# Performance work log

Measured on AMD Instinct MI355X. Metric: run time of the kernel, lower is better.

The kernel has to match this reference:

```python
import jax, jax.numpy as jnp
import numpy as np

B, S, E = 4, 2048, 1024
H, D = 16, 64

def setup_inputs() -> dict:
    key = jax.random.key(0)
    kx, kq, ko = jax.random.split(key, 3)
    scale_in = 1.0 / np.sqrt(E)
    scale_hd = 1.0 / np.sqrt(H * D)
    x = jax.random.normal(kx, (B, S, E), dtype=jnp.float32)
    W_qkv = jax.random.normal(kq, (E, 3, H, D), dtype=jnp.float32) * scale_in
    b_qkv = jnp.zeros((3, H, D), dtype=jnp.float32)
    W_out = jax.random.normal(ko, (H, D, E), dtype=jnp.float32) * scale_hd
    b_out = jnp.zeros((E,), dtype=jnp.float32)
    return {"x": x, "W_qkv": W_qkv, "b_qkv": b_qkv, "W_out": W_out, "b_out": b_out}

def reference(x, W_qkv, b_qkv, W_out, b_out):
    # QKV projection: [B,S,E] x [E,3,H,D] -> [B,S,3,H,D]
    qkv = jnp.einsum('bse,ethd->bsthd', x, W_qkv) + b_qkv
    q, k, v = qkv[:, :, 0], qkv[:, :, 1], qkv[:, :, 2]  # [B,S,H,D]
    # scores: [B,H,S(query),S(key)]
    scores = jnp.einsum('bqhd,bkhd->bhqk', q, k) / jnp.sqrt(jnp.float32(D))
    pos_q = jnp.arange(S)[:, None]
    pos_k = jnp.arange(S)[None, :]
    causal_mask = (pos_q >= pos_k).astype(scores.dtype)  # [S,S]
    scores = scores - 1e9 * (1.0 - causal_mask)
    weights = jax.nn.softmax(scores, axis=-1)
    # dropout is identity in inference mode
    answers = jnp.einsum('bhqk,bkhd->bqhd', weights, v)  # [B,S,H,D]
    out = jnp.einsum('bqhd,hde->bqe', answers, W_out) + b_out
    return out
```

## Files before the change

kernel.cpp:

```cpp
#include <hip/hip_runtime.h>
#include <math.h>

#define B_ 4
#define S_ 2048
#define E_ 1024
#define H_ 16
#define D_ 64

typedef _Float16 half8v __attribute__((ext_vector_type(8)));
typedef _Float16 half4v __attribute__((ext_vector_type(4)));
typedef __attribute__((ext_vector_type(4))) float f32x4;

__global__ __launch_bounds__(256)
void convert_f32_f16_kernel(const float* __restrict__ in, _Float16* __restrict__ out, int n4)
{
    const int i = blockIdx.x * 256 + threadIdx.x;
    if (i < n4) {
        float4 v = ((const float4*)in)[i];
        half4v h;
        h[0] = (_Float16)v.x; h[1] = (_Float16)v.y;
        h[2] = (_Float16)v.z; h[3] = (_Float16)v.w;
        ((half4v*)out)[i] = h;
    }
}

__global__ __launch_bounds__(256, 4)
void transpose_f32_f16_kernel(const float* __restrict__ in, _Float16* __restrict__ out,
                              int R, int C)
{
    __shared__ float tile[64][65];
    const int r0 = blockIdx.x * 64, c0 = blockIdx.y * 64;
    const int tr = threadIdx.x >> 6, tc = threadIdx.x & 63;
#pragma unroll
    for (int i = 0; i < 16; ++i)
        tile[i * 4 + tr][tc] = in[(size_t)(r0 + i * 4 + tr) * C + c0 + tc];
    __syncthreads();
#pragma unroll
    for (int i = 0; i < 16; ++i)
        out[(size_t)(c0 + i * 4 + tr) * R + r0 + tc] = (_Float16)tile[tc][i * 4 + tr];
}

__device__ __forceinline__ void gemm_core_f16(
    const _Float16* __restrict__ A, const _Float16* __restrict__ Bt,
    int bm, int bn, int tid,
    _Float16* As, _Float16* Bs,
    f32x4 (&acc)[4][4])
{
    const int K = 1024;
    const int lane = tid & 63;
    const int l15 = lane & 15, g = lane >> 4;
    const int w = tid >> 6;
    const int wm = (w >> 1) * 64, wn = (w & 1) * 64;
    const int swl = l15 & 7;

    const int sr = tid >> 3;
    const int sk = tid & 7;

    const _Float16* Ab = A + (size_t)(bm * 128) * K;
    const _Float16* Bb = Bt + (size_t)(bn * 128) * K;

    half8v arg[4], brg[4];
#pragma unroll
    for (int it = 0; it < 4; ++it) {
        arg[it] = *(const half8v*)(Ab + (size_t)(it * 32 + sr) * K + sk * 8);
        brg[it] = *(const half8v*)(Bb + (size_t)(it * 32 + sr) * K + sk * 8);
    }

    for (int k0 = 0; k0 < K; k0 += 64) {
        __syncthreads();
#pragma unroll
        for (int it = 0; it < 4; ++it) {
            const int r = it * 32 + sr;
            const int off = r * 64 + (sk ^ (r & 7)) * 8;
            *(half8v*)&As[off] = arg[it];
            *(half8v*)&Bs[off] = brg[it];
        }
        __syncthreads();
        if (k0 + 64 < K) {
#pragma unroll
            for (int it = 0; it < 4; ++it) {
                arg[it] = *(const half8v*)(Ab + (size_t)(it * 32 + sr) * K + k0 + 64 + sk * 8);
                brg[it] = *(const half8v*)(Bb + (size_t)(it * 32 + sr) * K + k0 + 64 + sk * 8);
            }
        }
#pragma unroll
        for (int kk = 0; kk < 2; ++kk) {
            const int slot = (kk * 4 + g) ^ swl;
            half8v af[4];
#pragma unroll
            for (int fm = 0; fm < 4; ++fm)
                af[fm] = *(const half8v*)&As[(wm + fm * 16 + l15) * 64 + slot * 8];
#pragma unroll
            for (int fn = 0; fn < 4; ++fn) {
                half8v bf = *(const half8v*)&Bs[(wn + fn * 16 + l15) * 64 + slot * 8];
#pragma unroll
                for (int fm = 0; fm < 4; ++fm)
                    acc[fm][fn] = __builtin_amdgcn_mfma_f32_16x16x32_f16(
                        af[fm], bf, acc[fm][fn], 0, 0, 0);
            }
        }
    }
}

__global__ __launch_bounds__(256, 2)
void gemm_qkv_f16_kernel(const _Float16* __restrict__ Xh, const _Float16* __restrict__ Wqh,
                         const float* __restrict__ bias,
                         _Float16* __restrict__ qf, _Float16* __restrict__ kf,
                         _Float16* __restrict__ vf)
{
    __shared__ _Float16 As[128 * 64], Bs[128 * 64];
    const int tid = threadIdx.x;
    const int bm = blockIdx.x, bn = blockIdx.y;

    f32x4 acc[4][4];
#pragma unroll
    for (int i = 0; i < 4; ++i)
#pragma unroll
        for (int j = 0; j < 4; ++j) acc[i][j] = f32x4{0.f, 0.f, 0.f, 0.f};

    gemm_core_f16(Xh, Wqh, bm, bn, tid, As, Bs, acc);

    const int lane = tid & 63;
    const int l15 = lane & 15, l4 = lane >> 4;
    const int w = tid >> 6;
    const int wm = (w >> 1) * 64, wn = (w & 1) * 64;

#pragma unroll
    for (int fn = 0; fn < 4; ++fn) {
        const int c = bn * 128 + wn + fn * 16 + l15;
        const float bv = bias[c];
        const int t = c >> 10;
        const int h = (c >> 6) & 15;
        const int d = c & 63;
        if (t < 2) {
            _Float16* dst = (t == 0) ? qf : kf;
#pragma unroll
            for (int fm = 0; fm < 4; ++fm) {
                const int rowb = bm * 128 + wm + fm * 16 + l4 * 4;
#pragma unroll
                for (int r = 0; r < 4; ++r) {
                    const int row = rowb + r;
                    const int b = row >> 11;
                    const int s = row & (S_ - 1);
                    dst[((size_t)(b * H_ + h) * S_ + s) * D_ + d] =
                        (_Float16)(acc[fm][fn][r] + bv);
                }
            }
        } else {
#pragma unroll
            for (int fm = 0; fm < 4; ++fm) {
                const int rowb = bm * 128 + wm + fm * 16 + l4 * 4;
                const int b = rowb >> 11;
                const int s0 = rowb & (S_ - 1);
                half4v pk;
#pragma unroll
                for (int r = 0; r < 4; ++r) pk[r] = (_Float16)(acc[fm][fn][r] + bv);
                *(half4v*)&vf[((size_t)(b * H_ + h) * D_ + d) * S_ + s0] = pk;
            }
        }
    }
}

__global__ __launch_bounds__(256, 4)
void flash_f16_kernel(const _Float16* __restrict__ qf, const _Float16* __restrict__ kf,
                      const _Float16* __restrict__ vf, _Float16* __restrict__ ansh)
{
    const int bh = blockIdx.y;
    const int b = bh >> 4, h = bh & 15;
    const int qb = (S_ / 64 - 1) - blockIdx.x;
    const int q0 = qb * 64;
    const int tid = threadIdx.x;
    const int lane = tid & 63;
    const int l15 = lane & 15, g = lane >> 4;
    const int w = tid >> 6;
    const int qrow = q0 + w * 16 + l15;
    const int swl = l15 & 7;

    __shared__ _Float16 Kh[64 * 64];
    __shared__ _Float16 Vth[64 * 64];

    half8v qh[2];
    {
        const _Float16* qp = qf + ((size_t)bh * S_ + qrow) * D_;
#pragma unroll
        for (int s = 0; s < 2; ++s) qh[s] = *(const half8v*)(qp + 32 * s + 8 * g);
    }

    f32x4 acc[4];
#pragma unroll
    for (int fd = 0; fd < 4; ++fd) acc[fd] = f32x4{0.f, 0.f, 0.f, 0.f};
    float m = -1e30f, lsum = 0.f;

    const int kp = tid & 63;
    const int kw = tid >> 6;
    const int vd = tid >> 2;
    const int vc = tid & 3;
    const int vbase = 32 * (vc >> 1) + 8 * (vc & 1);

    const _Float16* Kg = kf + (size_t)bh * S_ * D_;
    const _Float16* Vg = vf + ((size_t)bh * D_ + vd) * S_;

    const int nkv = qb + 1;

    half8v krA = *(const half8v*)(Kg + (size_t)kp * D_ + 16 * kw);
    half8v krB = *(const half8v*)(Kg + (size_t)kp * D_ + 16 * kw + 8);
    half8v vrA = *(const half8v*)(Vg + vbase);
    half8v vrB = *(const half8v*)(Vg + vbase + 16);

    for (int kb = 0; kb < nkv; ++kb) {
        const int k0 = kb * 64;
        __syncthreads();
        {
            const int o0 = kp * 64 + ((2 * kw) ^ (kp & 7)) * 8;
            const int o1 = kp * 64 + ((2 * kw + 1) ^ (kp & 7)) * 8;
            *(half8v*)&Kh[o0] = krA;
            *(half8v*)&Kh[o1] = krB;
            half8v c0, c1;
#pragma unroll
            for (int j = 0; j < 4; ++j) {
                c0[j] = vrA[j];     c0[4 + j] = vrB[j];
                c1[j] = vrA[4 + j]; c1[4 + j] = vrB[4 + j];
            }
            const int p0 = vd * 64 + ((2 * vc) ^ (vd & 7)) * 8;
            const int p1 = vd * 64 + ((2 * vc + 1) ^ (vd & 7)) * 8;
            *(half8v*)&Vth[p0] = c0;
            *(half8v*)&Vth[p1] = c1;
        }
        __syncthreads();
        if (kb + 1 < nkv) {
            const int kn = k0 + 64;
            krA = *(const half8v*)(Kg + (size_t)(kn + kp) * D_ + 16 * kw);
            krB = *(const half8v*)(Kg + (size_t)(kn + kp) * D_ + 16 * kw + 8);
            vrA = *(const half8v*)(Vg + kn + vbase);
            vrB = *(const half8v*)(Vg + kn + vbase + 16);
        }

        f32x4 qk[4];
#pragma unroll
        for (int f = 0; f < 4; ++f) qk[f] = f32x4{0.f, 0.f, 0.f, 0.f};
#pragma unroll
        for (int s = 0; s < 2; ++s) {
#pragma unroll
            for (int f = 0; f < 4; ++f) {
                const int off = (16 * f + l15) * 64 + ((4 * s + g) ^ swl) * 8;
                half8v kv = *(const half8v*)&Kh[off];
                qk[f] = __builtin_amdgcn_mfma_f32_16x16x32_f16(kv, qh[s], qk[f], 0, 0, 0);
            }
        }

        float p[4][4];
        float tmax = -1e30f;
#pragma unroll
        for (int f = 0; f < 4; ++f)
#pragma unroll
            for (int r = 0; r < 4; ++r) {
                const int kpos = k0 + 16 * f + 4 * g + r;
                float sv = qk[f][r] * 0.125f;
                sv = (kpos <= qrow) ? sv : -1e30f;
                p[f][r] = sv;
                tmax = fmaxf(tmax, sv);
            }
        tmax = fmaxf(tmax, __shfl_xor(tmax, 16));
        tmax = fmaxf(tmax, __shfl_xor(tmax, 32));
        const float mnew = fmaxf(m, tmax);
        const float corr = __expf(m - mnew);
#pragma unroll
        for (int fd = 0; fd < 4; ++fd) acc[fd] *= corr;
        float ls = 0.f;
#pragma unroll
        for (int f = 0; f < 4; ++f)
#pragma unroll
            for (int r = 0; r < 4; ++r) {
                const float e = __expf(p[f][r] - mnew);
                p[f][r] = e;
                ls += e;
            }
        ls += __shfl_xor(ls, 16);
        ls += __shfl_xor(ls, 32);
        lsum = lsum * corr + ls;
        m = mnew;

        half8v pb0, pb1;
#pragma unroll
        for (int j = 0; j < 4; ++j) {
            pb0[j]     = (_Float16)p[0][j];
            pb0[4 + j] = (_Float16)p[1][j];
            pb1[j]     = (_Float16)p[2][j];
            pb1[4 + j] = (_Float16)p[3][j];
        }

#pragma unroll
        for (int t = 0; t < 2; ++t) {
            const half8v pb = t ? pb1 : pb0;
#pragma unroll
            for (int fd = 0; fd < 4; ++fd) {
                const int off = (16 * fd + l15) * 64 + ((4 * t + g) ^ swl) * 8;
                half8v vv = *(const half8v*)&Vth[off];
                acc[fd] = __builtin_amdgcn_mfma_f32_16x16x32_f16(vv, pb, acc[fd], 0, 0, 0);
            }
        }
    }

    const float inv = 1.f / lsum;
    _Float16* dst = ansh + ((size_t)(b * S_ + qrow) * H_ + h) * D_;
#pragma unroll
    for (int fd = 0; fd < 4; ++fd) {
        half4v o4;
#pragma unroll
        for (int r = 0; r < 4; ++r) o4[r] = (_Float16)(acc[fd][r] * inv);
        *(half4v*)&dst[16 * fd + 4 * g] = o4;
    }
}

__global__ __launch_bounds__(256, 2)
void gemm_out_f16_kernel(const _Float16* __restrict__ Ah, const _Float16* __restrict__ Woh,
                         const float* __restrict__ bias, float* __restrict__ out)
{
    __shared__ _Float16 As[128 * 64], Bs[128 * 64];
    const int tid = threadIdx.x;
    const int bm = blockIdx.x, bn = blockIdx.y;

    f32x4 acc[4][4];
#pragma unroll
    for (int i = 0; i < 4; ++i)
#pragma unroll
        for (int j = 0; j < 4; ++j) acc[i][j] = f32x4{0.f, 0.f, 0.f, 0.f};

    gemm_core_f16(Ah, Woh, bm, bn, tid, As, Bs, acc);

    const int lane = tid & 63;
    const int l15 = lane & 15, l4 = lane >> 4;
    const int w = tid >> 6;
    const int wm = (w >> 1) * 64, wn = (w & 1) * 64;

#pragma unroll
    for (int fn = 0; fn < 4; ++fn) {
        const int c = bn * 128 + wn + fn * 16 + l15;
        const float bv = bias[c];
#pragma unroll
        for (int fm = 0; fm < 4; ++fm) {
            const int rowb = bm * 128 + wm + fm * 16 + l4 * 4;
#pragma unroll
            for (int r = 0; r < 4; ++r)
                out[(size_t)(rowb + r) * E_ + c] = acc[fm][fn][r] + bv;
        }
    }
}

extern "C" void kernel_launch(void* const* d_in, const int* in_sizes, int n_in,
                              void* d_out, int out_size, void* d_ws, size_t ws_size,
                              hipStream_t stream) {
    const float* x     = (const float*)d_in[0];
    const float* W_qkv = (const float*)d_in[1];
    const float* b_qkv = (const float*)d_in[2];
    const float* W_out = (const float*)d_in[3];
    const float* b_out = (const float*)d_in[4];
    float* out = (float*)d_out;

    const size_t N1 = (size_t)B_ * H_ * S_ * D_;
    const size_t MK = (size_t)8192 * 1024;
    const size_t WQ = (size_t)3072 * 1024;
    const size_t WO = (size_t)1024 * 1024;
    const size_t need = (MK + WQ + WO + 4 * N1) * sizeof(_Float16);
    if (ws_size < need) return;

    _Float16* Xh   = (_Float16*)d_ws;
    _Float16* Wqh  = Xh + MK;
    _Float16* Woh  = Wqh + WQ;
    _Float16* qf   = Woh + WO;
    _Float16* kf   = qf + N1;
    _Float16* vf   = kf + N1;
    _Float16* ansh = vf + N1;

    convert_f32_f16_kernel<<<(int)(MK / 4 / 256), 256, 0, stream>>>(x, Xh, (int)(MK / 4));
    transpose_f32_f16_kernel<<<dim3(16, 48), 256, 0, stream>>>(W_qkv, Wqh, 1024, 3072);
    transpose_f32_f16_kernel<<<dim3(16, 16), 256, 0, stream>>>(W_out, Woh, 1024, 1024);

    gemm_qkv_f16_kernel<<<dim3(64, 24), 256, 0, stream>>>(Xh, Wqh, b_qkv, qf, kf, vf);
    flash_f16_kernel<<<dim3(S_ / 64, B_ * H_), 256, 0, stream>>>(qf, kf, vf, ansh);
    gemm_out_f16_kernel<<<dim3(64, 8), 256, 0, stream>>>(ansh, Woh, b_out, out);
}
```

Measured before the change: 304.2 us.

## Pair causal query blocks per workgroup and double-buffer K/V tiles in flash kernel

Each flash-attention workgroup now handles two query blocks, j and 31-j, so every block does the same amount of causal work and each K/V tile loaded into shared memory is reused by both. K/V staging becomes double-buffered with one barrier per iteration. The online softmax skips rescaling when the new max rises by at most 8, and MFMA sections get raised wave priority. The costs are twice as many accumulator registers, double the LDS use, and a grid of only 1024 blocks, which could hurt occupancy.

```diff
diff --git a/kernel.cpp b/kernel.cpp
--- a/kernel.cpp
+++ b/kernel.cpp
@@ -161,35 +161,123 @@
     }
 }
 
+__device__ __forceinline__ void attn_tile(
+    const _Float16* __restrict__ Kb, const _Float16* __restrict__ Vb,
+    const half8v (&qh)[2], f32x4 (&acc)[4],
+    float& m, float& lsum,
+    int k0, int qrow, int l15, int g, int swl)
+{
+    f32x4 qk[4];
+#pragma unroll
+    for (int f = 0; f < 4; ++f) qk[f] = f32x4{0.f, 0.f, 0.f, 0.f};
+    __builtin_amdgcn_s_setprio(1);
+#pragma unroll
+    for (int s = 0; s < 2; ++s) {
+#pragma unroll
+        for (int f = 0; f < 4; ++f) {
+            const int off = (16 * f + l15) * 64 + ((4 * s + g) ^ swl) * 8;
+            half8v kv = *(const half8v*)&Kb[off];
+            qk[f] = __builtin_amdgcn_mfma_f32_16x16x32_f16(kv, qh[s], qk[f], 0, 0, 0);
+        }
+    }
+    __builtin_amdgcn_s_setprio(0);
+
+    float p[4][4];
+    float tmax = -1e30f;
+#pragma unroll
+    for (int f = 0; f < 4; ++f)
+#pragma unroll
+        for (int r = 0; r < 4; ++r) {
+            const int kpos = k0 + 16 * f + 4 * g + r;
+            float sv = qk[f][r] * 0.125f;
+            sv = (kpos <= qrow) ? sv : -1e30f;
+            p[f][r] = sv;
+            tmax = fmaxf(tmax, sv);
+        }
+    tmax = fmaxf(tmax, __shfl_xor(tmax, 16));
+    tmax = fmaxf(tmax, __shfl_xor(tmax, 32));
+
+    if (__ballot(tmax <= m + 8.f) != ~0ull) {
+        const float mnew = fmaxf(m, tmax);
+        const float corr = __expf(m - mnew);
+#pragma unroll
+        for (int fd = 0; fd < 4; ++fd) acc[fd] *= corr;
+        lsum *= corr;
+        m = mnew;
+    }
+    float ls = 0.f;
+#pragma unroll
+    for (int f = 0; f < 4; ++f)
+#pragma unroll
+        for (int r = 0; r < 4; ++r) {
+            const float e = __expf(p[f][r] - m);
+            p[f][r] = e;
+            ls += e;
+        }
+    ls += __shfl_xor(ls, 16);
+    ls += __shfl_xor(ls, 32);
+    lsum += ls;
+
+    half8v pb0, pb1;
+#pragma unroll
+    for (int jj = 0; jj < 4; ++jj) {
+        pb0[jj]     = (_Float16)p[0][jj];
+        pb0[4 + jj] = (_Float16)p[1][jj];
+        pb1[jj]     = (_Float16)p[2][jj];
+        pb1[4 + jj] = (_Float16)p[3][jj];
+    }
+
+    __builtin_amdgcn_s_setprio(1);
+#pragma unroll
+    for (int t = 0; t < 2; ++t) {
+        const half8v pb = t ? pb1 : pb0;
+#pragma unroll
+        for (int fd = 0; fd < 4; ++fd) {
+            const int off = (16 * fd + l15) * 64 + ((4 * t + g) ^ swl) * 8;
+            half8v vv = *(const half8v*)&Vb[off];
+            acc[fd] = __builtin_amdgcn_mfma_f32_16x16x32_f16(vv, pb, acc[fd], 0, 0, 0);
+        }
+    }
+    __builtin_amdgcn_s_setprio(0);
+}
+
 __global__ __launch_bounds__(256, 4)
 void flash_f16_kernel(const _Float16* __restrict__ qf, const _Float16* __restrict__ kf,
                       const _Float16* __restrict__ vf, _Float16* __restrict__ ansh)
 {
     const int bh = blockIdx.y;
     const int b = bh >> 4, h = bh & 15;
-    const int qb = (S_ / 64 - 1) - blockIdx.x;
-    const int q0 = qb * 64;
+    const int j  = blockIdx.x;
+    const int jb = 31 - j;
     const int tid = threadIdx.x;
     const int lane = tid & 63;
     const int l15 = lane & 15, g = lane >> 4;
     const int w = tid >> 6;
-    const int qrow = q0 + w * 16 + l15;
+    const int qrowA = j * 64 + w * 16 + l15;
+    const int qrowB = jb * 64 + w * 16 + l15;
     const int swl = l15 & 7;
 
-    __shared__ _Float16 Kh[64 * 64];
-    __shared__ _Float16 Vth[64 * 64];
-
-    half8v qh[2];
+    __shared__ _Float16 Kh[2][64 * 64];
+    __shared__ _Float16 Vth[2][64 * 64];
+
+    half8v qhA[2], qhB[2];
     {
-        const _Float16* qp = qf + ((size_t)bh * S_ + qrow) * D_;
-#pragma unroll
-        for (int s = 0; s < 2; ++s) qh[s] = *(const half8v*)(qp + 32 * s + 8 * g);
-    }
-
-    f32x4 acc[4];
-#pragma unroll
-    for (int fd = 0; fd < 4; ++fd) acc[fd] = f32x4{0.f, 0.f, 0.f, 0.f};
-    float m = -1e30f, lsum = 0.f;
+        const _Float16* qpA = qf + ((size_t)bh * S_ + qrowA) * D_;
+        const _Float16* qpB = qf + ((size_t)bh * S_ + qrowB) * D_;
+#pragma unroll
+        for (int s = 0; s < 2; ++s) {
+            qhA[s] = *(const half8v*)(qpA + 32 * s + 8 * g);
+            qhB[s] = *(const half8v*)(qpB + 32 * s + 8 * g);
+        }
+    }
+
+    f32x4 accA[4], accB[4];
+#pragma unroll
+    for (int fd = 0; fd < 4; ++fd) {
+        accA[fd] = f32x4{0.f, 0.f, 0.f, 0.f};
+        accB[fd] = f32x4{0.f, 0.f, 0.f, 0.f};
+    }
+    float mA = -1e30f, lAs = 0.f, mB = -1e30f, lBs = 0.f;
 
     const int kp = tid & 63;
     const int kw = tid >> 6;
@@ -200,115 +288,89 @@
     const _Float16* Kg = kf + (size_t)bh * S_ * D_;
     const _Float16* Vg = vf + ((size_t)bh * D_ + vd) * S_;
 
-    const int nkv = qb + 1;
-
-    half8v krA = *(const half8v*)(Kg + (size_t)kp * D_ + 16 * kw);
-    half8v krB = *(const half8v*)(Kg + (size_t)kp * D_ + 16 * kw + 8);
-    half8v vrA = *(const half8v*)(Vg + vbase);
-    half8v vrB = *(const half8v*)(Vg + vbase + 16);
+    const int nkv = jb + 1;
+
+    {
+        half8v kx0 = *(const half8v*)(Kg + (size_t)kp * D_ + 16 * kw);
+        half8v kx1 = *(const half8v*)(Kg + (size_t)kp * D_ + 16 * kw + 8);
+        half8v vx0 = *(const half8v*)(Vg + vbase);
+        half8v vx1 = *(const half8v*)(Vg + vbase + 16);
+        const int o0 = kp * 64 + ((2 * kw) ^ (kp & 7)) * 8;
+        const int o1 = kp * 64 + ((2 * kw + 1) ^ (kp & 7)) * 8;
+        *(half8v*)&Kh[0][o0] = kx0;
+        *(half8v*)&Kh[0][o1] = kx1;
+        half8v c0, c1;
+#pragma unroll
+        for (int jj = 0; jj < 4; ++jj) {
+            c0[jj] = vx0[jj];     c0[4 + jj] = vx1[jj];
+            c1[jj] = vx0[4 + jj]; c1[4 + jj] = vx1[4 + jj];
+        }
+        const int p0 = vd * 64 + ((2 * vc) ^ (vd & 7)) * 8;
+        const int p1 = vd * 64 + ((2 * vc + 1) ^ (vd & 7)) * 8;
+        *(half8v*)&Vth[0][p0] = c0;
+        *(half8v*)&Vth[0][p1] = c1;
+    }
+    __syncthreads();
 
     for (int kb = 0; kb < nkv; ++kb) {
+        const int cur = kb & 1;
         const int k0 = kb * 64;
-        __syncthreads();
-        {
+
+        half8v kx0, kx1, vx0, vx1;
+        const bool more = (kb + 1 < nkv);
+        if (more) {
+            const int kn = k0 + 64;
+            kx0 = *(const half8v*)(Kg + (size_t)(kn + kp) * D_ + 16 * kw);
+            kx1 = *(const half8v*)(Kg + (size_t)(kn + kp) * D_ + 16 * kw + 8);
+            vx0 = *(const half8v*)(Vg + kn + vbase);
+            vx1 = *(const half8v*)(Vg + kn + vbase + 16);
+        }
+
+        attn_tile(Kh[cur], Vth[cur], qhB, accB, mB, lBs, k0, qrowB, l15, g, swl);
+        if (kb <= j)
+            attn_tile(Kh[cur], Vth[cur], qhA, accA, mA, lAs, k0, qrowA, l15, g, swl);
+
+        if (more) {
+            const int nb = cur ^ 1;
             const int o0 = kp * 64 + ((2 * kw) ^ (kp & 7)) * 8;
             const int o1 = kp * 64 + ((2 * kw + 1) ^ (kp & 7)) * 8;
-            *(half8v*)&Kh[o0] = krA;
-            *(half8v*)&Kh[o1] = krB;
+            *(half8v*)&Kh[nb][o0] = kx0;
+            *(half8v*)&Kh[nb][o1] = kx1;
             half8v c0, c1;
 #pragma unroll
-            for (int j = 0; j < 4; ++j) {
-                c0[j] = vrA[j];     c0[4 + j] = vrB[j];
-                c1[j] = vrA[4 + j]; c1[4 + j] = vrB[4 + j];
+            for (int jj = 0; jj < 4; ++jj) {
+                c0[jj] = vx0[jj];     c0[4 + jj] = vx1[jj];
+                c1[jj] = vx0[4 + jj]; c1[4 + jj] = vx1[4 + jj];
             }
             const int p0 = vd * 64 + ((2 * vc) ^ (vd & 7)) * 8;
             const int p1 = vd * 64 + ((2 * vc + 1) ^ (vd & 7)) * 8;
-            *(half8v*)&Vth[p0] = c0;
-            *(half8v*)&Vth[p1] = c1;
+            *(half8v*)&Vth[nb][p0] = c0;
+            *(half8v*)&Vth[nb][p1] = c1;
         }
         __syncthreads();
-        if (kb + 1 < nkv) {
-            const int kn = k0 + 64;
-            krA = *(const half8v*)(Kg + (size_t)(kn + kp) * D_ + 16 * kw);
-            krB = *(const half8v*)(Kg + (size_t)(kn + kp) * D_ + 16 * kw + 8);
-            vrA = *(const half8v*)(Vg + kn + vbase);
-            vrB = *(const half8v*)(Vg + kn + vbase + 16);
-        }
-
-        f32x4 qk[4];
-#pragma unroll
-        for (int f = 0; f < 4; ++f) qk[f] = f32x4{0.f, 0.f, 0.f, 0.f};
-#pragma unroll
-        for (int s = 0; s < 2; ++s) {
-#pragma unroll
-            for (int f = 0; f < 4; ++f) {
-                const int off = (16 * f + l15) * 64 + ((4 * s + g) ^ swl) * 8;
-                half8v kv = *(const half8v*)&Kh[off];
-                qk[f] = __builtin_amdgcn_mfma_f32_16x16x32_f16(kv, qh[s], qk[f], 0, 0, 0);
-            }
-        }
-
-        float p[4][4];
-        float tmax = -1e30f;
-#pragma unroll
-        for (int f = 0; f < 4; ++f)
-#pragma unroll
-            for (int r = 0; r < 4; ++r) {
-                const int kpos = k0 + 16 * f + 4 * g + r;
-                float sv = qk[f][r] * 0.125f;
-                sv = (kpos <= qrow) ? sv : -1e30f;
-                p[f][r] = sv;
-                tmax = fmaxf(tmax, sv);
-            }
-        tmax = fmaxf(tmax, __shfl_xor(tmax, 16));
-        tmax = fmaxf(tmax, __shfl_xor(tmax, 32));
-        const float mnew = fmaxf(m, tmax);
-        const float corr = __expf(m - mnew);
-#pragma unroll
-        for (int fd = 0; fd < 4; ++fd) acc[fd] *= corr;
-        float ls = 0.f;
-#pragma unroll
-        for (int f = 0; f < 4; ++f)
-#pragma unroll
-            for (int r = 0; r < 4; ++r) {
-                const float e = __expf(p[f][r] - mnew);
-                p[f][r] = e;
-                ls += e;
-            }
-        ls += __shfl_xor(ls, 16);
-        ls += __shfl_xor(ls, 32);
-        lsum = lsum * corr + ls;
-        m = mnew;
-
-        half8v pb0, pb1;
-#pragma unroll
-        for (int j = 0; j < 4; ++j) {
-            pb0[j]     = (_Float16)p[0][j];
-            pb0[4 + j] = (_Float16)p[1][j];
-            pb1[j]     = (_Float16)p[2][j];
-            pb1[4 + j] = (_Float16)p[3][j];
-        }
-
-#pragma unroll
-        for (int t = 0; t < 2; ++t) {
-            const half8v pb = t ? pb1 : pb0;
-#pragma unroll
-            for (int fd = 0; fd < 4; ++fd) {
-                const int off = (16 * fd + l15) * 64 + ((4 * t + g) ^ swl) * 8;
-                half8v vv = *(const half8v*)&Vth[off];
-                acc[fd] = __builtin_amdgcn_mfma_f32_16x16x32_f16(vv, pb, acc[fd], 0, 0, 0);
-            }
-        }
-    }
-
-    const float inv = 1.f / lsum;
-    _Float16* dst = ansh + ((size_t)(b * S_ + qrow) * H_ + h) * D_;
-#pragma unroll
-    for (int fd = 0; fd < 4; ++fd) {
-        half4v o4;
-#pragma unroll
-        for (int r = 0; r < 4; ++r) o4[r] = (_Float16)(acc[fd][r] * inv);
-        *(half4v*)&dst[16 * fd + 4 * g] = o4;
+    }
+
+    {
+        const float inv = 1.f / lAs;
+        _Float16* dst = ansh + ((size_t)(b * S_ + qrowA) * H_ + h) * D_;
+#pragma unroll
+        for (int fd = 0; fd < 4; ++fd) {
+            half4v o4;
+#pragma unroll
+            for (int r = 0; r < 4; ++r) o4[r] = (_Float16)(accA[fd][r] * inv);
+            *(half4v*)&dst[16 * fd + 4 * g] = o4;
+        }
+    }
+    {
+        const float inv = 1.f / lBs;
+        _Float16* dst = ansh + ((size_t)(b * S_ + qrowB) * H_ + h) * D_;
+#pragma unroll
+        for (int fd = 0; fd < 4; ++fd) {
+            half4v o4;
+#pragma unroll
+            for (int r = 0; r < 4; ++r) o4[r] = (_Float16)(accB[fd][r] * inv);
+            *(half4v*)&dst[16 * fd + 4 * g] = o4;
+        }
     }
 }
 
@@ -377,6 +439,6 @@
     transpose_f32_f16_kernel<<<dim3(16, 16), 256, 0, stream>>>(W_out, Woh, 1024, 1024);
 
     gemm_qkv_f16_kernel<<<dim3(64, 24), 256, 0, stream>>>(Xh, Wqh, b_qkv, qf, kf, vf);
-    flash_f16_kernel<<<dim3(S_ / 64, B_ * H_), 256, 0, stream>>>(qf, kf, vf, ansh);
+    flash_f16_kernel<<<dim3(16, B_ * H_), 256, 0, stream>>>(qf, kf, vf, ansh);
     gemm_out_f16_kernel<<<dim3(64, 8), 256, 0, stream>>>(ansh, Woh, b_out, out);
 }
```

Measured after the change: 287.6 us. 1.06x faster.
